# Kernel optimization log

Hardware: AMD Instinct MI355X
Metric: run time of the kernel (lower is better)

The kernel has to match this reference:

```python
import jax, jax.numpy as jnp
import numpy as np

LATENT = 256

def setup_inputs() -> dict:
    key = jax.random.key(0)
    k1, k2, k3, k4, k5 = jax.random.split(key, 5)
    B, Te, Td, D = 4, 512, 256, LATENT
    encoder_output = jax.random.normal(k1, (B, Te, D), dtype=jnp.float32)
    decoder_output = jax.random.normal(k2, (B, Td, D), dtype=jnp.float32)
    # 'random_normal' keras initializer: stddev 0.05
    W_a = jax.random.normal(k3, (D, D), dtype=jnp.float32) * 0.05
    U_a = jax.random.normal(k4, (D, D), dtype=jnp.float32) * 0.05
    V_a = jax.random.normal(k5, (D, 1), dtype=jnp.float32) * 0.05
    return {"encoder_output": encoder_output, "decoder_output": decoder_output,
            "W_a": W_a, "U_a": U_a, "V_a": V_a}

def reference(encoder_output, decoder_output, W_a, U_a, V_a):
    # Projections computed once per position (mathematically equal to the
    # tiled tensordots in the original, without redundant GEMM work).
    W_enc = jnp.einsum('bed,df->bef', encoder_output, W_a)   # [B,Te,D]
    U_dec = jnp.einsum('btd,df->btf', decoder_output, U_a)   # [B,Td,D]
    # Broadcast add replaces the explicit tf.tile: [B,Td,Te,D]
    e = jnp.tanh(W_enc[:, None, :, :] + U_dec[:, :, None, :])
    score = jnp.einsum('bted,do->bte', e, V_a[:, 0:1])        # [B,Td,Te]
    attention_weights = jax.nn.softmax(score, axis=-1)
    context_vector = jnp.einsum('bte,bed->btd', attention_weights, encoder_output)
    return (context_vector, attention_weights)
```

## Files before the change

### kernel.cpp

```cpp
#include <hip/hip_runtime.h>

#define B 4
#define TE 512
#define TD 256
#define D 256

#define C2    2.8853900817779268f
#define LOG2E 1.4426950408889634f

__device__ __forceinline__ void qcomb4(float& q, const float4& v,
                                       float p0, float p1, float p2, float p3)
{
    const float n01 = fmaf(v.y, p0, v.x * p1);
    const float d01 = p0 * p1;
    const float n23 = fmaf(v.w, p2, v.z * p3);
    const float d23 = p2 * p3;
    const float num = fmaf(n23, d01, n01 * d23);
    const float den = d01 * d23;
    q = fmaf(num, __builtin_amdgcn_rcpf(den), q);
}

__device__ __forceinline__ void score4(float& q, const float4& v4,
                                       const float4& w, const float4& a)
{
    qcomb4(q, v4, fmaf(w.x, a.x, 1.0f), fmaf(w.y, a.y, 1.0f),
                  fmaf(w.z, a.z, 1.0f), fmaf(w.w, a.w, 1.0f));
}

__global__ __launch_bounds__(256) void proj_kernel(
    const float* __restrict__ enc, const float* __restrict__ Wa,
    float* __restrict__ ewt)
{
    __shared__ float a_lds[8 * 256];
    const int tid = threadIdx.x;
    const int blk = blockIdx.x;
    const int xcd = blk & 7;
    const int b   = xcd >> 1;
    const int j   = ((xcd & 1) << 5) | (blk >> 3);
    const int e0  = j * 8;

    {
        const float4* src = (const float4*)(enc + ((size_t)(b * 512 + e0)) * 256);
        ((float4*)a_lds)[tid]       = src[tid];
        ((float4*)a_lds)[tid + 256] = src[tid + 256];
    }
    __syncthreads();

    float acc[8] = {0.f,0.f,0.f,0.f,0.f,0.f,0.f,0.f};

    #pragma unroll 4
    for (int k = 0; k < 256; k += 4) {
        const float w0 = Wa[(k + 0) * 256 + tid];
        const float w1 = Wa[(k + 1) * 256 + tid];
        const float w2 = Wa[(k + 2) * 256 + tid];
        const float w3 = Wa[(k + 3) * 256 + tid];
        #pragma unroll
        for (int r = 0; r < 8; r++) {
            const float4 a4 = *(const float4*)&a_lds[r * 256 + k];
            acc[r] = fmaf(a4.x, w0, acc[r]);
            acc[r] = fmaf(a4.y, w1, acc[r]);
            acc[r] = fmaf(a4.z, w2, acc[r]);
            acc[r] = fmaf(a4.w, w3, acc[r]);
        }
    }

    float* o = ewt + (((size_t)(b * 64 + (tid >> 2)) * 512 + e0) << 2) + (tid & 3);
    #pragma unroll
    for (int r = 0; r < 8; r++)
        o[r * 4] = __builtin_amdgcn_exp2f(acc[r] * C2);
}

__global__ __launch_bounds__(1024) void attn_kernel(
    const float* __restrict__ enc, const float* __restrict__ dec,
    const float* __restrict__ Ua,  const float* __restrict__ Va,
    const float* __restrict__ ewt,
    float* __restrict__ ctx, float* __restrict__ aw)
{
    __shared__ float eul[4 * 256];
    __shared__ float val[256];
    __shared__ float decl[4 * 256];
    __shared__ float sc[4][TE];
    __shared__ float wred[2][4][4];
    __shared__ float part[4][4][256];

    const int tid = threadIdx.x;
    const int blk = blockIdx.x;
    const int xcd = blk & 7;
    const int b   = xcd >> 1;
    const int tq  = ((xcd & 1) << 5) | (blk >> 3);
    const int t0  = tq * 4;
    const int bt0 = b * 256 + t0;

    float* const scratch = &part[0][0][0];

    if (tid < 256) val[tid] = Va[tid];
    decl[tid] = dec[(size_t)bt0 * 256 + tid];
    __syncthreads();

    {
        const int dg = tid & 63;
        const int t  = (tid >> 6) & 3;
        const int kq = tid >> 8;
        const float4* Ua4 = (const float4*)Ua;
        const float*  dr  = &decl[t * 256];
        float4 a4 = make_float4(0.f, 0.f, 0.f, 0.f);
        #pragma unroll 4
        for (int i = 0; i < 64; ++i) {
            const int k = kq * 64 + i;
            const float  dv = dr[k];
            const float4 u4 = Ua4[k * 64 + dg];
            a4.x = fmaf(dv, u4.x, a4.x);
            a4.y = fmaf(dv, u4.y, a4.y);
            a4.z = fmaf(dv, u4.z, a4.z);
            a4.w = fmaf(dv, u4.w, a4.w);
        }
        ((float4*)scratch)[(kq * 4 + t) * 64 + dg] = a4;
    }
    __syncthreads();
    {
        const float s = scratch[tid] + scratch[1024 + tid] +
                        scratch[2048 + tid] + scratch[3072 + tid];
        eul[tid] = __builtin_amdgcn_exp2f(s * C2);
    }
    __syncthreads();

    {
        const int e  = tid & 511;
        const int tp = tid >> 9;
        const float4* __restrict__ ewb =
            (const float4*)ewt + (size_t)(b * 64 + tp * 32) * 512 + e;
        float q0 = 0.f, q1 = 0.f, q2 = 0.f, q3 = 0.f;

        #pragma unroll 2
        for (int it = 0; it < 16; ++it) {
            const float4 w0 = ewb[(it * 2 + 0) * 512];
            const float4 w1 = ewb[(it * 2 + 1) * 512];
            const int d0 = (tp * 32 + it * 2) * 4;
            {
                const float4 v4 = *(const float4*)&val[d0];
                score4(q0, v4, w0, *(const float4*)&eul[      d0]);
                score4(q1, v4, w0, *(const float4*)&eul[256 + d0]);
                score4(q2, v4, w0, *(const float4*)&eul[512 + d0]);
                score4(q3, v4, w0, *(const float4*)&eul[768 + d0]);
            }
            {
                const int d1 = d0 + 4;
                const float4 v4 = *(const float4*)&val[d1];
                score4(q0, v4, w1, *(const float4*)&eul[      d1]);
                score4(q1, v4, w1, *(const float4*)&eul[256 + d1]);
                score4(q2, v4, w1, *(const float4*)&eul[512 + d1]);
                score4(q3, v4, w1, *(const float4*)&eul[768 + d1]);
            }
        }

        if (tp) {
            scratch[       e] = q0;
            scratch[512  + e] = q1;
            scratch[1024 + e] = q2;
            scratch[1536 + e] = q3;
        }
        __syncthreads();
        if (!tp) {
            sc[0][e] = -2.0f * (q0 + scratch[       e]);
            sc[1][e] = -2.0f * (q1 + scratch[512  + e]);
            sc[2][e] = -2.0f * (q2 + scratch[1024 + e]);
            sc[3][e] = -2.0f * (q3 + scratch[1536 + e]);
        }
    }
    __syncthreads();

    {
        const int wv   = tid >> 6;
        const int lane = tid & 63;
        const int t    = wv >> 2;
        const int seg  = wv & 3;
        float* __restrict__ srow = &sc[t][seg * 128];

        const float x0 = srow[lane];
        const float x1 = srow[lane + 64];

        float m = fmaxf(x0, x1);
        #pragma unroll
        for (int s = 32; s > 0; s >>= 1) m = fmaxf(m, __shfl_xor(m, s, 64));
        if (lane == 0) wred[0][t][seg] = m;
        __syncthreads();
        const float4 mm = *(const float4*)&wred[0][t][0];
        const float M = fmaxf(fmaxf(mm.x, mm.y), fmaxf(mm.z, mm.w));

        const float g0 = __builtin_amdgcn_exp2f((x0 - M) * LOG2E);
        const float g1 = __builtin_amdgcn_exp2f((x1 - M) * LOG2E);

        float ssum = g0 + g1;
        #pragma unroll
        for (int s = 32; s > 0; s >>= 1) ssum += __shfl_xor(ssum, s, 64);
        if (lane == 0) wred[1][t][seg] = ssum;
        __syncthreads();
        const float4 sm = *(const float4*)&wred[1][t][0];
        const float inv = __builtin_amdgcn_rcpf((sm.x + sm.y) + (sm.z + sm.w));

        const float p0 = g0 * inv, p1 = g1 * inv;
        srow[lane]      = p0;
        srow[lane + 64] = p1;
        float* __restrict__ ao = aw + ((size_t)(bt0 + t)) * 512 + seg * 128;
        ao[lane]      = p0;
        ao[lane + 64] = p1;
    }
    __syncthreads();

    {
        const int eg = tid >> 8;
        const int dl = tid & 255;
        const float* __restrict__ eb =
            enc + ((size_t)b * 512 + eg * 128) * 256 + dl;
        const int e0 = eg * 128;

        float c0 = 0.f, c1 = 0.f, c2 = 0.f, c3 = 0.f;
        #pragma unroll 4
        for (int jj = 0; jj < 128; jj += 4) {
            const float4 w0 = *(const float4*)&sc[0][e0 + jj];
            const float4 w1 = *(const float4*)&sc[1][e0 + jj];
            const float4 w2 = *(const float4*)&sc[2][e0 + jj];
            const float4 w3 = *(const float4*)&sc[3][e0 + jj];
            const float r0 = eb[(jj + 0) * 256];
            const float r1 = eb[(jj + 1) * 256];
            const float r2 = eb[(jj + 2) * 256];
            const float r3 = eb[(jj + 3) * 256];
            c0 = fmaf(w0.x, r0, c0); c0 = fmaf(w0.y, r1, c0); c0 = fmaf(w0.z, r2, c0); c0 = fmaf(w0.w, r3, c0);
            c1 = fmaf(w1.x, r0, c1); c1 = fmaf(w1.y, r1, c1); c1 = fmaf(w1.z, r2, c1); c1 = fmaf(w1.w, r3, c1);
            c2 = fmaf(w2.x, r0, c2); c2 = fmaf(w2.y, r1, c2); c2 = fmaf(w2.z, r2, c2); c2 = fmaf(w2.w, r3, c2);
            c3 = fmaf(w3.x, r0, c3); c3 = fmaf(w3.y, r1, c3); c3 = fmaf(w3.z, r2, c3); c3 = fmaf(w3.w, r3, c3);
        }
        part[eg][0][dl] = c0;
        part[eg][1][dl] = c1;
        part[eg][2][dl] = c2;
        part[eg][3][dl] = c3;
    }
    __syncthreads();

    {
        const int t  = tid >> 8;
        const int dl = tid & 255;
        ctx[((size_t)(bt0 + t)) * 256 + dl] =
            (part[0][t][dl] + part[1][t][dl]) +
            (part[2][t][dl] + part[3][t][dl]);
    }
}

extern "C" void kernel_launch(void* const* d_in, const int* in_sizes, int n_in,
                              void* d_out, int out_size, void* d_ws, size_t ws_size,
                              hipStream_t stream) {
    const float* enc = (const float*)d_in[0];
    const float* dec = (const float*)d_in[1];
    const float* Wa  = (const float*)d_in[2];
    const float* Ua  = (const float*)d_in[3];
    const float* Va  = (const float*)d_in[4];

    float* out = (float*)d_out;
    float* ctx = out;
    float* aw  = out + B * TD * D;

    float* ewt = (float*)d_ws;

    proj_kernel<<<dim3(256), dim3(256),  0, stream>>>(enc, Wa, ewt);
    attn_kernel<<<dim3(256), dim3(1024), 0, stream>>>(enc, dec, Ua, Va, ewt, ctx, aw);
}
```

Before: 110.7 us.

## Move decoder U_a projection from attention kernel into projection kernel

The decoder projection exp(2*dec·U_a) is now computed in the projection kernel alongside the encoder projection, using 512 threads per block, and written to a workspace buffer. The attention kernel then loads the precomputed values instead of running its own small GEMM, two syncs and a reduction. This shortens the attention kernel's prologue at the cost of more work and an extra write/read of a B×Td×D buffer in the first kernel.

```diff
diff --git a/kernel.cpp b/kernel.cpp
--- a/kernel.cpp
+++ b/kernel.cpp
@@ -27,58 +27,90 @@
                   fmaf(w.z, a.z, 1.0f), fmaf(w.w, a.w, 1.0f));
 }
 
-__global__ __launch_bounds__(256) void proj_kernel(
-    const float* __restrict__ enc, const float* __restrict__ Wa,
-    float* __restrict__ ewt)
+__global__ __launch_bounds__(512) void proj_kernel(
+    const float* __restrict__ enc, const float* __restrict__ dec,
+    const float* __restrict__ Wa,  const float* __restrict__ Ua,
+    float* __restrict__ ewt, float* __restrict__ eu)
 {
     __shared__ float a_lds[8 * 256];
+    __shared__ float d_lds[4 * 256];
+
     const int tid = threadIdx.x;
     const int blk = blockIdx.x;
     const int xcd = blk & 7;
     const int b   = xcd >> 1;
     const int j   = ((xcd & 1) << 5) | (blk >> 3);
     const int e0  = j * 8;
-
-    {
-        const float4* src = (const float4*)(enc + ((size_t)(b * 512 + e0)) * 256);
-        ((float4*)a_lds)[tid]       = src[tid];
-        ((float4*)a_lds)[tid + 256] = src[tid + 256];
-    }
-    __syncthreads();
-
-    float acc[8] = {0.f,0.f,0.f,0.f,0.f,0.f,0.f,0.f};
+    const int t0  = j * 4;
+
+    {
+        const float4* esrc = (const float4*)(enc + ((size_t)(b * 512 + e0)) * 256);
+        ((float4*)a_lds)[tid] = esrc[tid];
+        if (tid < 256) {
+            const float4* dsrc = (const float4*)(dec + ((size_t)(b * 256 + t0)) * 256);
+            ((float4*)d_lds)[tid] = dsrc[tid];
+        }
+    }
+    __syncthreads();
+
+    const int d = tid & 255;
+    const int h = tid >> 8;
+    const float* __restrict__ arow = a_lds + (4 * h) * 256;
+    const float* __restrict__ drow = d_lds + (2 * h) * 256;
+
+    float acc[4]  = {0.f, 0.f, 0.f, 0.f};
+    float dacc[2] = {0.f, 0.f};
 
     #pragma unroll 4
     for (int k = 0; k < 256; k += 4) {
-        const float w0 = Wa[(k + 0) * 256 + tid];
-        const float w1 = Wa[(k + 1) * 256 + tid];
-        const float w2 = Wa[(k + 2) * 256 + tid];
-        const float w3 = Wa[(k + 3) * 256 + tid];
-        #pragma unroll
-        for (int r = 0; r < 8; r++) {
-            const float4 a4 = *(const float4*)&a_lds[r * 256 + k];
+        const float w0 = Wa[(k + 0) * 256 + d];
+        const float w1 = Wa[(k + 1) * 256 + d];
+        const float w2 = Wa[(k + 2) * 256 + d];
+        const float w3 = Wa[(k + 3) * 256 + d];
+        const float u0 = Ua[(k + 0) * 256 + d];
+        const float u1 = Ua[(k + 1) * 256 + d];
+        const float u2 = Ua[(k + 2) * 256 + d];
+        const float u3 = Ua[(k + 3) * 256 + d];
+        #pragma unroll
+        for (int r = 0; r < 4; r++) {
+            const float4 a4 = *(const float4*)&arow[r * 256 + k];
             acc[r] = fmaf(a4.x, w0, acc[r]);
             acc[r] = fmaf(a4.y, w1, acc[r]);
             acc[r] = fmaf(a4.z, w2, acc[r]);
             acc[r] = fmaf(a4.w, w3, acc[r]);
         }
-    }
-
-    float* o = ewt + (((size_t)(b * 64 + (tid >> 2)) * 512 + e0) << 2) + (tid & 3);
-    #pragma unroll
-    for (int r = 0; r < 8; r++)
-        o[r * 4] = __builtin_amdgcn_exp2f(acc[r] * C2);
+        #pragma unroll
+        for (int r = 0; r < 2; r++) {
+            const float4 d4 = *(const float4*)&drow[r * 256 + k];
+            dacc[r] = fmaf(d4.x, u0, dacc[r]);
+            dacc[r] = fmaf(d4.y, u1, dacc[r]);
+            dacc[r] = fmaf(d4.z, u2, dacc[r]);
+            dacc[r] = fmaf(d4.w, u3, dacc[r]);
+        }
+    }
+
+    {
+        float* o = ewt + (((size_t)(b * 64 + (d >> 2)) * 512 + e0 + 4 * h) << 2)
+                       + (d & 3);
+        #pragma unroll
+        for (int r = 0; r < 4; r++)
+            o[r * 4] = __builtin_amdgcn_exp2f(acc[r] * C2);
+    }
+    {
+        #pragma unroll
+        for (int r = 0; r < 2; r++)
+            eu[(size_t)(b * 256 + t0 + 2 * h + r) * 256 + d] =
+                __builtin_amdgcn_exp2f(dacc[r] * C2);
+    }
 }
 
 __global__ __launch_bounds__(1024) void attn_kernel(
-    const float* __restrict__ enc, const float* __restrict__ dec,
-    const float* __restrict__ Ua,  const float* __restrict__ Va,
-    const float* __restrict__ ewt,
+    const float* __restrict__ enc, const float* __restrict__ ewt,
+    const float* __restrict__ eu,  const float* __restrict__ Va,
     float* __restrict__ ctx, float* __restrict__ aw)
 {
     __shared__ float eul[4 * 256];
     __shared__ float val[256];
-    __shared__ float decl[4 * 256];
     __shared__ float sc[4][TE];
     __shared__ float wred[2][4][4];
     __shared__ float part[4][4][256];
@@ -94,34 +126,7 @@
     float* const scratch = &part[0][0][0];
 
     if (tid < 256) val[tid] = Va[tid];
-    decl[tid] = dec[(size_t)bt0 * 256 + tid];
-    __syncthreads();
-
-    {
-        const int dg = tid & 63;
-        const int t  = (tid >> 6) & 3;
-        const int kq = tid >> 8;
-        const float4* Ua4 = (const float4*)Ua;
-        const float*  dr  = &decl[t * 256];
-        float4 a4 = make_float4(0.f, 0.f, 0.f, 0.f);
-        #pragma unroll 4
-        for (int i = 0; i < 64; ++i) {
-            const int k = kq * 64 + i;
-            const float  dv = dr[k];
-            const float4 u4 = Ua4[k * 64 + dg];
-            a4.x = fmaf(dv, u4.x, a4.x);
-            a4.y = fmaf(dv, u4.y, a4.y);
-            a4.z = fmaf(dv, u4.z, a4.z);
-            a4.w = fmaf(dv, u4.w, a4.w);
-        }
-        ((float4*)scratch)[(kq * 4 + t) * 64 + dg] = a4;
-    }
-    __syncthreads();
-    {
-        const float s = scratch[tid] + scratch[1024 + tid] +
-                        scratch[2048 + tid] + scratch[3072 + tid];
-        eul[tid] = __builtin_amdgcn_exp2f(s * C2);
-    }
+    eul[tid] = eu[(size_t)bt0 * 256 + tid];
     __syncthreads();
 
     {
@@ -260,7 +265,8 @@
     float* aw  = out + B * TD * D;
 
     float* ewt = (float*)d_ws;
-
-    proj_kernel<<<dim3(256), dim3(256),  0, stream>>>(enc, Wa, ewt);
-    attn_kernel<<<dim3(256), dim3(1024), 0, stream>>>(enc, dec, Ua, Va, ewt, ctx, aw);
-}
+    float* eu  = ewt + (size_t)B * D * TE;
+
+    proj_kernel<<<dim3(256), dim3(512),  0, stream>>>(enc, dec, Wa, Ua, ewt, eu);
+    attn_kernel<<<dim3(256), dim3(1024), 0, stream>>>(enc, ewt, eu, Va, ctx, aw);
+}
```

After: 167.5 us. 1.51x slower.

## Move decoder projection into proj kernel as extra blocks

Applied to the files above, without the earlier changes.

The decoder projection (dec·U_a followed by exp2) was computed inside each attention block from a per-block LDS staging step and a split-K reduction. It now runs in the projection kernel as 128 extra blocks that write exp(2·U_dec) to a workspace buffer, and the attention kernel just loads it. This removes two syncs and a GEMM phase from the attention kernel's prologue, at the cost of an extra global round-trip and a larger first grid.

```diff
diff --git a/kernel.cpp b/kernel.cpp
--- a/kernel.cpp
+++ b/kernel.cpp
@@ -28,19 +28,33 @@
 }
 
 __global__ __launch_bounds__(256) void proj_kernel(
-    const float* __restrict__ enc, const float* __restrict__ Wa,
-    float* __restrict__ ewt)
+    const float* __restrict__ enc, const float* __restrict__ dec,
+    const float* __restrict__ Wa,  const float* __restrict__ Ua,
+    float* __restrict__ ewt, float* __restrict__ eu)
 {
     __shared__ float a_lds[8 * 256];
     const int tid = threadIdx.x;
     const int blk = blockIdx.x;
-    const int xcd = blk & 7;
-    const int b   = xcd >> 1;
-    const int j   = ((xcd & 1) << 5) | (blk >> 3);
-    const int e0  = j * 8;
-
-    {
-        const float4* src = (const float4*)(enc + ((size_t)(b * 512 + e0)) * 256);
+    const bool is_enc = blk < 256;
+    const float* __restrict__ A = is_enc ? enc : dec;
+    const float* __restrict__ W = is_enc ? Wa  : Ua;
+
+    int row0;
+    if (is_enc) {
+        const int xcd = blk & 7;
+        const int b   = xcd >> 1;
+        const int j   = ((xcd & 1) << 5) | (blk >> 3);
+        row0 = b * 512 + j * 8;
+    } else {
+        const int blk2 = blk - 256;
+        const int xcd  = blk2 & 7;
+        const int b    = xcd >> 1;
+        const int j    = ((xcd & 1) << 4) | (blk2 >> 3);
+        row0 = b * 256 + j * 8;
+    }
+
+    {
+        const float4* src = (const float4*)(A + (size_t)row0 * 256);
         ((float4*)a_lds)[tid]       = src[tid];
         ((float4*)a_lds)[tid + 256] = src[tid + 256];
     }
@@ -50,10 +64,10 @@
 
     #pragma unroll 4
     for (int k = 0; k < 256; k += 4) {
-        const float w0 = Wa[(k + 0) * 256 + tid];
-        const float w1 = Wa[(k + 1) * 256 + tid];
-        const float w2 = Wa[(k + 2) * 256 + tid];
-        const float w3 = Wa[(k + 3) * 256 + tid];
+        const float w0 = W[(k + 0) * 256 + tid];
+        const float w1 = W[(k + 1) * 256 + tid];
+        const float w2 = W[(k + 2) * 256 + tid];
+        const float w3 = W[(k + 3) * 256 + tid];
         #pragma unroll
         for (int r = 0; r < 8; r++) {
             const float4 a4 = *(const float4*)&a_lds[r * 256 + k];
@@ -64,21 +78,33 @@
         }
     }
 
-    float* o = ewt + (((size_t)(b * 64 + (tid >> 2)) * 512 + e0) << 2) + (tid & 3);
+    float f[8];
     #pragma unroll
     for (int r = 0; r < 8; r++)
-        o[r * 4] = __builtin_amdgcn_exp2f(acc[r] * C2);
+        f[r] = __builtin_amdgcn_exp2f(acc[r] * C2);
+
+    if (is_enc) {
+        const int b  = row0 >> 9;
+        const int e0 = row0 & 511;
+        float* o = ewt + (((size_t)(b * 64 + (tid >> 2)) * 512 + e0) << 2)
+                       + (tid & 3);
+        #pragma unroll
+        for (int r = 0; r < 8; r++)
+            o[r * 4] = f[r];
+    } else {
+        #pragma unroll
+        for (int r = 0; r < 8; r++)
+            eu[(size_t)(row0 + r) * 256 + tid] = f[r];
+    }
 }
 
 __global__ __launch_bounds__(1024) void attn_kernel(
-    const float* __restrict__ enc, const float* __restrict__ dec,
-    const float* __restrict__ Ua,  const float* __restrict__ Va,
-    const float* __restrict__ ewt,
+    const float* __restrict__ enc, const float* __restrict__ ewt,
+    const float* __restrict__ eu,  const float* __restrict__ Va,
     float* __restrict__ ctx, float* __restrict__ aw)
 {
     __shared__ float eul[4 * 256];
     __shared__ float val[256];
-    __shared__ float decl[4 * 256];
     __shared__ float sc[4][TE];
     __shared__ float wred[2][4][4];
     __shared__ float part[4][4][256];
@@ -94,34 +120,7 @@
     float* const scratch = &part[0][0][0];
 
     if (tid < 256) val[tid] = Va[tid];
-    decl[tid] = dec[(size_t)bt0 * 256 + tid];
-    __syncthreads();
-
-    {
-        const int dg = tid & 63;
-        const int t  = (tid >> 6) & 3;
-        const int kq = tid >> 8;
-        const float4* Ua4 = (const float4*)Ua;
-        const float*  dr  = &decl[t * 256];
-        float4 a4 = make_float4(0.f, 0.f, 0.f, 0.f);
-        #pragma unroll 4
-        for (int i = 0; i < 64; ++i) {
-            const int k = kq * 64 + i;
-            const float  dv = dr[k];
-            const float4 u4 = Ua4[k * 64 + dg];
-            a4.x = fmaf(dv, u4.x, a4.x);
-            a4.y = fmaf(dv, u4.y, a4.y);
-            a4.z = fmaf(dv, u4.z, a4.z);
-            a4.w = fmaf(dv, u4.w, a4.w);
-        }
-        ((float4*)scratch)[(kq * 4 + t) * 64 + dg] = a4;
-    }
-    __syncthreads();
-    {
-        const float s = scratch[tid] + scratch[1024 + tid] +
-                        scratch[2048 + tid] + scratch[3072 + tid];
-        eul[tid] = __builtin_amdgcn_exp2f(s * C2);
-    }
+    eul[tid] = eu[(size_t)bt0 * 256 + tid];
     __syncthreads();
 
     {
@@ -260,7 +259,8 @@
     float* aw  = out + B * TD * D;
 
     float* ewt = (float*)d_ws;
-
-    proj_kernel<<<dim3(256), dim3(256),  0, stream>>>(enc, Wa, ewt);
-    attn_kernel<<<dim3(256), dim3(1024), 0, stream>>>(enc, dec, Ua, Va, ewt, ctx, aw);
-}
+    float* eu  = ewt + (size_t)B * D * TE;
+
+    proj_kernel<<<dim3(384), dim3(256), 0, stream>>>(enc, dec, Wa, Ua, ewt, eu);
+    attn_kernel<<<dim3(256), dim3(1024), 0, stream>>>(enc, ewt, eu, Va, ctx, aw);
+}
```

Result: faster. 105.6 us (-4.5%).
